# Kernel optimization log

Hardware: AMD Instinct MI355X
Metric: run time of the kernel (lower is better)

Reference implementation:

```python
import jax, jax.numpy as jnp
import numpy as np

B = 16384
EMBED = 1536
DETER = 1024
STOC = 32
HID = 1024
ACT = 12
DIST = 2 * STOC  # mean + std
EPS_LN = 1e-3


def _ln(x, g, b):
    m = jnp.mean(x, axis=-1, keepdims=True)
    v = jnp.mean((x - m) ** 2, axis=-1, keepdims=True)
    return (x - m) * jax.lax.rsqrt(v + EPS_LN) * g + b


def _lin(x, w, b=None):
    y = x @ w.T
    return y if b is None else y + b


def setup_inputs() -> dict:
    key = jax.random.key(0)
    ks = jax.random.split(key, 24)

    def w(k, o, i):
        return jax.random.normal(k, (o, i), jnp.float32) / np.sqrt(i)

    inp = {
        "embedding": jax.random.normal(ks[0], (B, EMBED), jnp.float32),
        "action": jax.random.normal(ks[1], (B, ACT), jnp.float32),
        "mask": jnp.ones((B, 1), jnp.float32),
        "deter": jax.random.normal(ks[2], (B, DETER), jnp.float32),
        "stoc": jax.random.normal(ks[3], (B, STOC), jnp.float32),
        # pre_gru: Linear(stoc+act -> hid)
        "w_pre": w(ks[4], HID, STOC + ACT),
        "b_pre": jnp.zeros((HID,), jnp.float32),
        # NormGRUCell (no bias on ih/hh)
        "w_ih": w(ks[5], 3 * DETER, HID),
        "w_hh": w(ks[6], 3 * DETER, DETER),
        "ln_r_g": jnp.ones((DETER,), jnp.float32), "ln_r_b": jnp.zeros((DETER,), jnp.float32),
        "ln_u_g": jnp.ones((DETER,), jnp.float32), "ln_u_b": jnp.zeros((DETER,), jnp.float32),
        "ln_n_g": jnp.ones((DETER,), jnp.float32), "ln_n_b": jnp.zeros((DETER,), jnp.float32),
        # prior MLP (model_idx = 0)
        "wp1": w(ks[7], HID, DETER), "bp1": jnp.zeros((HID,), jnp.float32),
        "wp2": w(ks[8], DIST, HID), "bp2": jnp.zeros((DIST,), jnp.float32),
        # post MLP
        "wq1": w(ks[9], HID, DETER + EMBED), "bq1": jnp.zeros((HID,), jnp.float32),
        "wq2": w(ks[10], DIST, HID), "bq2": jnp.zeros((DIST,), jnp.float32),
    }
    return inp


def reference(embedding, action, mask, deter, stoc,
              w_pre, b_pre, w_ih, w_hh,
              ln_r_g, ln_r_b, ln_u_g, ln_u_b, ln_n_g, ln_n_b,
              wp1, bp1, wp2, bp2, wq1, bq1, wq2, bq2):
    deter = deter * mask
    stoc = stoc * mask
    x = jax.nn.relu(_lin(jnp.concatenate([stoc, action], -1), w_pre, b_pre))

    # LayerNorm GRU cell
    gi = x @ w_ih.T          # [B, 3*DETER]
    gh = deter @ w_hh.T      # [B, 3*DETER]
    ri, ui, ni = jnp.split(gi, 3, axis=1)
    rh, uh, nh = jnp.split(gh, 3, axis=1)
    reset = jax.nn.sigmoid(_ln(ri + rh, ln_r_g, ln_r_b))
    update = jax.nn.sigmoid(_ln(ui + uh, ln_u_g, ln_u_b))
    newval = jnp.tanh(_ln(ni + reset * nh, ln_n_g, ln_n_b))
    h = update * newval + (1.0 - update) * deter  # [B, DETER]

    # prior head (model 0)
    prior = _lin(jax.nn.relu(_lin(h, wp1, bp1)), wp2, bp2)
    prior_mean, prior_std = jnp.split(prior, 2, axis=-1)
    prior_std = jax.nn.softplus(prior_std) + 0.1

    # posterior head
    post = _lin(jax.nn.relu(_lin(jnp.concatenate([h, embedding], -1), wq1, bq1)), wq2, bq2)
    post_mean, post_std = jnp.split(post, 2, axis=-1)
    post_std = jax.nn.softplus(post_std) + 0.1

    post_latent = post_mean  # sample=False -> Normal mean
    return (post_mean, post_std, prior_mean, prior_std, h, post_latent)
```

## Files before the change

kernel.cpp:

```cpp
#include <hip/hip_runtime.h>
#include <hip/hip_bf16.h>
#include <cstdint>

#define BB 16384

typedef __attribute__((ext_vector_type(8))) short short8;
typedef __attribute__((ext_vector_type(4))) float f32x4;

__device__ __forceinline__ unsigned short f2bf(float x) {
    uint32_t u = __float_as_uint(x);
    u += 0x7FFFu + ((u >> 16) & 1u);
    return (unsigned short)(u >> 16);
}
__device__ __forceinline__ float bf2f(unsigned short b) {
    return __uint_as_float(((uint32_t)b) << 16);
}
__device__ __forceinline__ void split2(float x, unsigned short* hi, unsigned short* lo) {
    unsigned short h = f2bf(x);
    *hi = h;
    *lo = f2bf(x - bf2f(h));
}

#define GLL(gp, lp) __builtin_amdgcn_global_load_lds( \
    (const __attribute__((address_space(1))) void*)(gp), \
    (__attribute__((address_space(3))) void*)(lp), 16, 0, 0)


__global__ __launch_bounds__(256) void split_sa(
    const float* __restrict__ stoc, const float* __restrict__ action,
    const float* __restrict__ mask,
    unsigned short* __restrict__ hi, unsigned short* __restrict__ lo) {
    int tid = threadIdx.x;
    int r = blockIdx.x * 4 + (tid >> 6);
    int c = tid & 63;
    float v = 0.f;
    if (c < 32) v = stoc[(size_t)r * 32 + c] * mask[r];
    else if (c < 44) v = action[(size_t)r * 12 + (c - 32)];
    size_t o = (size_t)r * 64 + c;
    unsigned short h, l; split2(v, &h, &l);
    hi[o] = h; lo[o] = l;
}

__global__ __launch_bounds__(256) void split_wpre(
    const float* __restrict__ w, unsigned short* __restrict__ hi, unsigned short* __restrict__ lo) {
    int idx = blockIdx.x * 256 + threadIdx.x;
    int row = idx >> 6, c = idx & 63;
    float v = (c < 44) ? w[row * 44 + c] : 0.f;
    unsigned short h, l; split2(v, &h, &l);
    hi[idx] = h; lo[idx] = l;
}

__global__ __launch_bounds__(256) void split_weights(
    const float* __restrict__ w0, unsigned short* __restrict__ h0, unsigned short* __restrict__ l0,
    const float* __restrict__ w1, unsigned short* __restrict__ h1, unsigned short* __restrict__ l1,
    const float* __restrict__ w2, unsigned short* __restrict__ h2, unsigned short* __restrict__ l2,
    const float* __restrict__ w3, unsigned short* __restrict__ h3, unsigned short* __restrict__ l3) {
    int b = blockIdx.x;
    const float* src; unsigned short* hi; unsigned short* lo; int lb;
    if (b < 3072)      { src = w0; hi = h0; lo = l0; lb = b; }
    else if (b < 6144) { src = w1; hi = h1; lo = l1; lb = b - 3072; }
    else if (b < 7168) { src = w2; hi = h2; lo = l2; lb = b - 6144; }
    else               { src = w3; hi = h3; lo = l3; lb = b - 7168; }
    size_t i4 = (size_t)lb * 256 + threadIdx.x;
    float4 v = ((const float4*)src)[i4];
    ushort4 h, l;
    split2(v.x, &h.x, &l.x);
    split2(v.y, &h.y, &l.y);
    split2(v.z, &h.z, &l.z);
    split2(v.w, &h.w, &l.w);
    ((ushort4*)hi)[i4] = h;
    ((ushort4*)lo)[i4] = l;
}

__global__ __launch_bounds__(256) void split_embed(
    const float* __restrict__ e, unsigned short* __restrict__ hi, unsigned short* __restrict__ lo) {
    int b = blockIdx.y;
    int c = blockIdx.x * 256 + threadIdx.x;
    float v = e[(size_t)b * 1536 + c];
    size_t o = (size_t)b * 2560 + 1024 + c;
    unsigned short h, l; split2(v, &h, &l);
    hi[o] = h; lo[o] = l;
}

__global__ __launch_bounds__(256) void split_deter(
    const float* __restrict__ dt, const float* __restrict__ mask,
    unsigned short* __restrict__ hi, unsigned short* __restrict__ lo) {
    int b = blockIdx.y;
    int c = blockIdx.x * 256 + threadIdx.x;
    float v = dt[(size_t)b * 1024 + c] * mask[b];
    size_t o = (size_t)b * 1024 + c;
    unsigned short h, l; split2(v, &h, &l);
    hi[o] = h; lo[o] = l;
}

template<int RELU, int BF16OUT, int ACC>
__global__ __launch_bounds__(256, 3) void gemm_hl(
    const unsigned short* __restrict__ Ahi, const unsigned short* __restrict__ Alo, int lda,
    const unsigned short* __restrict__ Bhi, const unsigned short* __restrict__ Blo, int ldb,
    const float* __restrict__ bias,
    float* __restrict__ Cf, unsigned short* __restrict__ Chi, unsigned short* __restrict__ Clo,
    int ldc, int K, int nbn, int gm) {
    __shared__ unsigned short lsAh[128 * 32], lsAl[128 * 32];
    __shared__ unsigned short lsBh[128 * 32], lsBl[128 * 32];

    const int tid = threadIdx.x;
    const int wave = tid >> 6, lane = tid & 63;

    int bid = blockIdx.x;
    int group = bid / (gm * nbn);
    int rem = bid % (gm * nbn);
    int bm = group * gm + (rem % gm);
    int bn = rem / gm;
    const int m0 = bm * 128, n0 = bn * 128;

    const int wm = (wave >> 1) * 64, wn = (wave & 1) * 64;
    const int lr = lane & 15;
    const int ka = (((lane >> 4) ^ ((lane >> 1) & 3)) * 8);

    const int srow = tid >> 2;
    const int scol = (((tid & 3) ^ ((tid >> 3) & 3)) * 8);
    const unsigned short* gA0h = Ahi + (size_t)(m0 + srow) * lda + scol;
    const unsigned short* gA1h = gA0h + (size_t)64 * lda;
    const unsigned short* gA0l = Alo + (size_t)(m0 + srow) * lda + scol;
    const unsigned short* gA1l = gA0l + (size_t)64 * lda;
    const unsigned short* gB0h = Bhi + (size_t)(n0 + srow) * ldb + scol;
    const unsigned short* gB1h = gB0h + (size_t)64 * ldb;
    const unsigned short* gB0l = Blo + (size_t)(n0 + srow) * ldb + scol;
    const unsigned short* gB1l = gB0l + (size_t)64 * ldb;
    const int lds0 = wave * 512;
    const int lds1 = 2048 + wave * 512;

    f32x4 acc[4][4];
    #pragma unroll
    for (int i = 0; i < 4; i++)
        #pragma unroll
        for (int j = 0; j < 4; j++) acc[i][j] = (f32x4){0.f, 0.f, 0.f, 0.f};

    for (int k = 0; k < K; k += 32) {
        __syncthreads();
        GLL(gA0h + k, &lsAh[lds0]);
        GLL(gA1h + k, &lsAh[lds1]);
        GLL(gA0l + k, &lsAl[lds0]);
        GLL(gA1l + k, &lsAl[lds1]);
        GLL(gB0h + k, &lsBh[lds0]);
        GLL(gB1h + k, &lsBh[lds1]);
        GLL(gB0l + k, &lsBl[lds0]);
        GLL(gB1l + k, &lsBl[lds1]);
        __syncthreads();

        short8 a_[4], b_[4], t_[4];
        #pragma unroll
        for (int i = 0; i < 4; i++) {
            a_[i] = *(const short8*)&lsAh[(wm + i * 16 + lr) * 32 + ka];
            b_[i] = *(const short8*)&lsBh[(wn + i * 16 + lr) * 32 + ka];
        }
        #pragma unroll
        for (int i = 0; i < 4; i++)
            #pragma unroll
            for (int j = 0; j < 4; j++)
                acc[i][j] = __builtin_amdgcn_mfma_f32_16x16x32_bf16(a_[i], b_[j], acc[i][j], 0, 0, 0);
        #pragma unroll
        for (int i = 0; i < 4; i++) t_[i] = *(const short8*)&lsBl[(wn + i * 16 + lr) * 32 + ka];
        #pragma unroll
        for (int i = 0; i < 4; i++)
            #pragma unroll
            for (int j = 0; j < 4; j++)
                acc[i][j] = __builtin_amdgcn_mfma_f32_16x16x32_bf16(a_[i], t_[j], acc[i][j], 0, 0, 0);
        #pragma unroll
        for (int i = 0; i < 4; i++) a_[i] = *(const short8*)&lsAl[(wm + i * 16 + lr) * 32 + ka];
        #pragma unroll
        for (int i = 0; i < 4; i++)
            #pragma unroll
            for (int j = 0; j < 4; j++)
                acc[i][j] = __builtin_amdgcn_mfma_f32_16x16x32_bf16(a_[i], b_[j], acc[i][j], 0, 0, 0);
    }

    const int orow = m0 + wm + (lane >> 4) * 4;
    const int ocol = n0 + wn + lr;
    #pragma unroll
    for (int j = 0; j < 4; j++) {
        int col = ocol + j * 16;
        float bv = bias ? bias[col] : 0.f;
        #pragma unroll
        for (int i = 0; i < 4; i++) {
            #pragma unroll
            for (int q = 0; q < 4; q++) {
                int row = orow + i * 16 + q;
                float x = acc[i][j][q] + bv;
                if (ACC) x += Cf[(size_t)row * ldc + col];
                if (RELU) x = fmaxf(x, 0.f);
                if (BF16OUT) {
                    unsigned short h_, l_; split2(x, &h_, &l_);
                    Chi[(size_t)row * ldc + col] = h_;
                    Clo[(size_t)row * ldc + col] = l_;
                } else {
                    Cf[(size_t)row * ldc + col] = x;
                }
            }
        }
    }
}

__device__ __forceinline__ float block_sum(float v, float* red, int tid) {
    #pragma unroll
    for (int m = 32; m >= 1; m >>= 1) v += __shfl_xor(v, m, 64);
    __syncthreads();
    if ((tid & 63) == 0) red[tid >> 6] = v;
    __syncthreads();
    return red[0] + red[1] + red[2] + red[3];
}

__global__ __launch_bounds__(256) void ln_gru(
    const float* __restrict__ gsum, const float* __restrict__ ginb,
    const float* __restrict__ deter, const float* __restrict__ mask,
    const float* __restrict__ grg, const float* __restrict__ grb,
    const float* __restrict__ gug, const float* __restrict__ gub,
    const float* __restrict__ gng, const float* __restrict__ gnb,
    float* __restrict__ hout, unsigned short* __restrict__ hehi, unsigned short* __restrict__ helo) {
    __shared__ float red[4];
    const int b = blockIdx.x, tid = threadIdx.x;
    const float* gr = gsum + (size_t)b * 3072;
    const float mk = mask[b];
    float r[4], u[4], gin[4], ghn[4], dm[4];
    int c[4];
    #pragma unroll
    for (int j = 0; j < 4; j++) {
        c[j] = tid + 256 * j;
        r[j] = gr[c[j]];
        u[j] = gr[1024 + c[j]];
        ghn[j] = gr[2048 + c[j]];
        gin[j] = ginb[(size_t)b * 1024 + c[j]];
        dm[j] = deter[(size_t)b * 1024 + c[j]] * mk;
    }
    const float inv = 1.f / 1024.f;

    float mr = block_sum(r[0] + r[1] + r[2] + r[3], red, tid) * inv;
    float vr;
    {
        float d0 = r[0] - mr, d1 = r[1] - mr, d2 = r[2] - mr, d3 = r[3] - mr;
        vr = block_sum(d0 * d0 + d1 * d1 + d2 * d2 + d3 * d3, red, tid) * inv;
    }
    float sr = rsqrtf(vr + 1e-3f);
    float reset[4];
    #pragma unroll
    for (int j = 0; j < 4; j++) {
        float y = (r[j] - mr) * sr * grg[c[j]] + grb[c[j]];
        reset[j] = 1.f / (1.f + expf(-y));
    }

    float mu = block_sum(u[0] + u[1] + u[2] + u[3], red, tid) * inv;
    float vu;
    {
        float d0 = u[0] - mu, d1 = u[1] - mu, d2 = u[2] - mu, d3 = u[3] - mu;
        vu = block_sum(d0 * d0 + d1 * d1 + d2 * d2 + d3 * d3, red, tid) * inv;
    }
    float su = rsqrtf(vu + 1e-3f);
    float upd[4];
    #pragma unroll
    for (int j = 0; j < 4; j++) {
        float y = (u[j] - mu) * su * gug[c[j]] + gub[c[j]];
        upd[j] = 1.f / (1.f + expf(-y));
    }

    float nin[4];
    #pragma unroll
    for (int j = 0; j < 4; j++) nin[j] = gin[j] + reset[j] * ghn[j];
    float mn = block_sum(nin[0] + nin[1] + nin[2] + nin[3], red, tid) * inv;
    float vn;
    {
        float d0 = nin[0] - mn, d1 = nin[1] - mn, d2 = nin[2] - mn, d3 = nin[3] - mn;
        vn = block_sum(d0 * d0 + d1 * d1 + d2 * d2 + d3 * d3, red, tid) * inv;
    }
    float sn = rsqrtf(vn + 1e-3f);
    #pragma unroll
    for (int j = 0; j < 4; j++) {
        float y = (nin[j] - mn) * sn * gng[c[j]] + gnb[c[j]];
        float nv = tanhf(y);
        float h = upd[j] * nv + (1.f - upd[j]) * dm[j];
        hout[(size_t)b * 1024 + c[j]] = h;
        unsigned short hh, hl; split2(h, &hh, &hl);
        size_t o = (size_t)b * 2560 + c[j];
        hehi[o] = hh;
        helo[o] = hl;
    }
}

__global__ __launch_bounds__(256) void head2(
    const unsigned short* __restrict__ ahi, const unsigned short* __restrict__ alo,
    const float* __restrict__ w, const float* __restrict__ bias,
    float* __restrict__ omean, float* __restrict__ ostd, float* __restrict__ olat) {
    __shared__ float arow[8 * 1024];
    const int tid = threadIdx.x;
    const size_t base = (size_t)blockIdx.x * 8 * 1024;
    for (int i = tid; i < 8 * 1024; i += 256)
        arow[i] = bf2f(ahi[base + i]) + bf2f(alo[base + i]);
    __syncthreads();

    const int j = tid & 63, rq = tid >> 6;
    float acc0 = 0.f, acc1 = 0.f;
    const float* wr = w + (size_t)j * 1024;
    for (int k = 0; k < 1024; k += 4) {
        float4 wv = *(const float4*)(wr + k);
        const float* a0 = &arow[rq * 1024 + k];
        const float* a1 = &arow[(rq + 4) * 1024 + k];
        acc0 += a0[0] * wv.x + a0[1] * wv.y + a0[2] * wv.z + a0[3] * wv.w;
        acc1 += a1[0] * wv.x + a1[1] * wv.y + a1[2] * wv.z + a1[3] * wv.w;
    }
    const float bv = bias[j];
    const int rbase = blockIdx.x * 8;
    float accs[2] = {acc0, acc1};
    #pragma unroll
    for (int t = 0; t < 2; t++) {
        int row = rbase + rq + 4 * t;
        float val = accs[t] + bv;
        if (j < 32) {
            omean[(size_t)row * 32 + j] = val;
            if (olat) olat[(size_t)row * 32 + j] = val;
        } else {
            float sp = fmaxf(val, 0.f) + log1pf(expf(-fabsf(val))) + 0.1f;
            ostd[(size_t)row * 32 + (j - 32)] = sp;
        }
    }
}

static inline size_t rup(size_t x) { return (x + 255) & ~(size_t)255; }

extern "C" void kernel_launch(void* const* d_in, const int* in_sizes, int n_in,
                              void* d_out, int out_size, void* d_ws, size_t ws_size,
                              hipStream_t stream) {
    const float* embedding = (const float*)d_in[0];
    const float* action    = (const float*)d_in[1];
    const float* mask      = (const float*)d_in[2];
    const float* deter     = (const float*)d_in[3];
    const float* stoc      = (const float*)d_in[4];
    const float* w_pre     = (const float*)d_in[5];
    const float* b_pre     = (const float*)d_in[6];
    const float* w_ih      = (const float*)d_in[7];
    const float* w_hh      = (const float*)d_in[8];
    const float* ln_r_g    = (const float*)d_in[9];
    const float* ln_r_b    = (const float*)d_in[10];
    const float* ln_u_g    = (const float*)d_in[11];
    const float* ln_u_b    = (const float*)d_in[12];
    const float* ln_n_g    = (const float*)d_in[13];
    const float* ln_n_b    = (const float*)d_in[14];
    const float* wp1       = (const float*)d_in[15];
    const float* bp1       = (const float*)d_in[16];
    const float* wp2       = (const float*)d_in[17];
    const float* bp2       = (const float*)d_in[18];
    const float* wq1       = (const float*)d_in[19];
    const float* bq1       = (const float*)d_in[20];
    const float* wq2       = (const float*)d_in[21];
    const float* bq2       = (const float*)d_in[22];
    float* out = (float*)d_out;

    const size_t wbytes =
        2 * rup((size_t)65536 * 2) +
        4 * rup((size_t)3072 * 1024 * 2) +
        2 * rup((size_t)1024 * 1024 * 2) +
        2 * rup((size_t)1024 * 2560 * 2);
    int NCH = 16;
    {
        const int cands[5] = {1, 2, 4, 8, 16};
        for (int ci = 0; ci < 5; ci++) {
            size_t Bc = (size_t)BB / cands[ci];
            size_t need = wbytes + Bc * 30976 + (1u << 20);
            if (need <= ws_size) { NCH = cands[ci]; break; }
        }
    }
    const int Bc = BB / NCH;
    const int nbm = Bc / 128;
    const int gm = nbm < 32 ? nbm : 32;

    char* p = (char*)d_ws;
    auto alloc = [&](size_t bytes) { char* r = p; p += rup(bytes); return r; };
    unsigned short* wpre_hi = (unsigned short*)alloc((size_t)65536 * 2);
    unsigned short* wpre_lo = (unsigned short*)alloc((size_t)65536 * 2);
    unsigned short* wih_hi  = (unsigned short*)alloc((size_t)3072 * 1024 * 2);
    unsigned short* wih_lo  = (unsigned short*)alloc((size_t)3072 * 1024 * 2);
    unsigned short* whh_hi  = (unsigned short*)alloc((size_t)3072 * 1024 * 2);
    unsigned short* whh_lo  = (unsigned short*)alloc((size_t)3072 * 1024 * 2);
    unsigned short* wp1_hi  = (unsigned short*)alloc((size_t)1024 * 1024 * 2);
    unsigned short* wp1_lo  = (unsigned short*)alloc((size_t)1024 * 1024 * 2);
    unsigned short* wq1_hi  = (unsigned short*)alloc((size_t)1024 * 2560 * 2);
    unsigned short* wq1_lo  = (unsigned short*)alloc((size_t)1024 * 2560 * 2);
    unsigned short* sa_hi   = (unsigned short*)alloc((size_t)Bc * 64 * 2);
    unsigned short* sa_lo   = (unsigned short*)alloc((size_t)Bc * 64 * 2);
    unsigned short* xh      = (unsigned short*)alloc((size_t)Bc * 1024 * 2);
    unsigned short* xl      = (unsigned short*)alloc((size_t)Bc * 1024 * 2);
    unsigned short* dh      = (unsigned short*)alloc((size_t)Bc * 1024 * 2);
    unsigned short* dl      = (unsigned short*)alloc((size_t)Bc * 1024 * 2);
    float* gh_buf           = (float*)alloc((size_t)Bc * 3072 * 4);
    unsigned short* he_hi   = (unsigned short*)alloc((size_t)Bc * 2560 * 2);
    unsigned short* he_lo   = (unsigned short*)alloc((size_t)Bc * 2560 * 2);
    (void)dl;
    float* gin = (float*)dh;
    unsigned short* p1_hi = (unsigned short*)gh_buf;
    unsigned short* p1_lo = p1_hi + (size_t)Bc * 1024;
    unsigned short* q1_hi = p1_lo + (size_t)Bc * 1024;
    unsigned short* q1_lo = q1_hi + (size_t)Bc * 1024;

    split_wpre<<<256, 256, 0, stream>>>(w_pre, wpre_hi, wpre_lo);
    split_weights<<<9728, 256, 0, stream>>>(
        w_ih, wih_hi, wih_lo, w_hh, whh_hi, whh_lo,
        wp1, wp1_hi, wp1_lo, wq1, wq1_hi, wq1_lo);

    for (int ch = 0; ch < NCH; ch++) {
        const size_t r0 = (size_t)ch * Bc;

        split_sa<<<Bc / 4, 256, 0, stream>>>(
            stoc + r0 * 32, action + r0 * 12, mask + r0, sa_hi, sa_lo);
        split_embed<<<dim3(6, Bc), 256, 0, stream>>>(
            embedding + r0 * 1536, he_hi, he_lo);
        split_deter<<<dim3(4, Bc), 256, 0, stream>>>(
            deter + r0 * 1024, mask + r0, dh, dl);

        gemm_hl<1, 1, 0><<<nbm * 8, 256, 0, stream>>>(
            sa_hi, sa_lo, 64, wpre_hi, wpre_lo, 64, b_pre,
            nullptr, xh, xl, 1024, 64, 8, gm);

        gemm_hl<0, 0, 0><<<nbm * 24, 256, 0, stream>>>(
            dh, dl, 1024, whh_hi, whh_lo, 1024, nullptr,
            gh_buf, nullptr, nullptr, 3072, 1024, 24, gm);

        gemm_hl<0, 0, 1><<<nbm * 16, 256, 0, stream>>>(
            xh, xl, 1024, wih_hi, wih_lo, 1024, nullptr,
            gh_buf, nullptr, nullptr, 3072, 1024, 16, gm);

        gemm_hl<0, 0, 0><<<nbm * 8, 256, 0, stream>>>(
            xh, xl, 1024, wih_hi + (size_t)2048 * 1024, wih_lo + (size_t)2048 * 1024, 1024,
            nullptr, gin, nullptr, nullptr, 1024, 1024, 8, gm);

        ln_gru<<<Bc, 256, 0, stream>>>(
            gh_buf, gin, deter + r0 * 1024, mask + r0,
            ln_r_g, ln_r_b, ln_u_g, ln_u_b, ln_n_g, ln_n_b,
            out + (size_t)BB * 128 + r0 * 1024, he_hi, he_lo);

        gemm_hl<1, 1, 0><<<nbm * 8, 256, 0, stream>>>(
            he_hi, he_lo, 2560, wp1_hi, wp1_lo, 1024, bp1,
            nullptr, p1_hi, p1_lo, 1024, 1024, 8, gm);

        gemm_hl<1, 1, 0><<<nbm * 8, 256, 0, stream>>>(
            he_hi, he_lo, 2560, wq1_hi, wq1_lo, 2560, bq1,
            nullptr, q1_hi, q1_lo, 1024, 2560, 8, gm);

        head2<<<Bc / 8, 256, 0, stream>>>(p1_hi, p1_lo, wp2, bp2,
            out + (size_t)BB * 64 + r0 * 32, out + (size_t)BB * 96 + r0 * 32, nullptr);
        head2<<<Bc / 8, 256, 0, stream>>>(q1_hi, q1_lo, wq2, bq2,
            out + r0 * 32, out + (size_t)BB * 32 + r0 * 32,
            out + (size_t)BB * 1152 + r0 * 32);
    }
}
```

Measured before the change: 1.968 ms.

## Use 256x128 tiles with 8 waves and triple-buffered LDS prefetch pipeline

Replaces the 128x128, 4-wave split-bf16 GEMM with a 256x128 tile run by 8 waves. LDS is triple-buffered, and global-to-LDS loads for step t+2 are issued in between the MFMA phases of step t. Fewer, finer-grained barriers and s_setprio are used around the MFMA blocks so that memory traffic overlaps compute, and the larger tile improves data reuse. The cost is a much larger LDS footprint (about 144KB per block), which limits occupancy. Correctness also depends on the vmcnt bookkeeping being right.

```diff
diff --git a/kernel.cpp b/kernel.cpp
--- a/kernel.cpp
+++ b/kernel.cpp
@@ -94,14 +94,13 @@
 }
 
 template<int RELU, int BF16OUT, int ACC>
-__global__ __launch_bounds__(256, 3) void gemm_hl(
+__global__ __launch_bounds__(512, 2) void gemm_mp(
     const unsigned short* __restrict__ Ahi, const unsigned short* __restrict__ Alo, int lda,
     const unsigned short* __restrict__ Bhi, const unsigned short* __restrict__ Blo, int ldb,
     const float* __restrict__ bias,
     float* __restrict__ Cf, unsigned short* __restrict__ Chi, unsigned short* __restrict__ Clo,
     int ldc, int K, int nbn, int gm) {
-    __shared__ unsigned short lsAh[128 * 32], lsAl[128 * 32];
-    __shared__ unsigned short lsBh[128 * 32], lsBl[128 * 32];
+    __shared__ unsigned short sm[3 * 24576];
 
     const int tid = threadIdx.x;
     const int wave = tid >> 6, lane = tid & 63;
@@ -111,7 +110,7 @@
     int rem = bid % (gm * nbn);
     int bm = group * gm + (rem % gm);
     int bn = rem / gm;
-    const int m0 = bm * 128, n0 = bn * 128;
+    const int m0 = bm * 256, n0 = bn * 128;
 
     const int wm = (wave >> 1) * 64, wn = (wave & 1) * 64;
     const int lr = lane & 15;
@@ -120,15 +119,13 @@
     const int srow = tid >> 2;
     const int scol = (((tid & 3) ^ ((tid >> 3) & 3)) * 8);
     const unsigned short* gA0h = Ahi + (size_t)(m0 + srow) * lda + scol;
-    const unsigned short* gA1h = gA0h + (size_t)64 * lda;
+    const unsigned short* gA1h = gA0h + (size_t)128 * lda;
     const unsigned short* gA0l = Alo + (size_t)(m0 + srow) * lda + scol;
-    const unsigned short* gA1l = gA0l + (size_t)64 * lda;
+    const unsigned short* gA1l = gA0l + (size_t)128 * lda;
     const unsigned short* gB0h = Bhi + (size_t)(n0 + srow) * ldb + scol;
-    const unsigned short* gB1h = gB0h + (size_t)64 * ldb;
     const unsigned short* gB0l = Blo + (size_t)(n0 + srow) * ldb + scol;
-    const unsigned short* gB1l = gB0l + (size_t)64 * ldb;
-    const int lds0 = wave * 512;
-    const int lds1 = 2048 + wave * 512;
+
+    const int wofs = wave * 512;
 
     f32x4 acc[4][4];
     #pragma unroll
@@ -136,43 +133,83 @@
         #pragma unroll
         for (int j = 0; j < 4; j++) acc[i][j] = (f32x4){0.f, 0.f, 0.f, 0.f};
 
-    for (int k = 0; k < K; k += 32) {
-        __syncthreads();
-        GLL(gA0h + k, &lsAh[lds0]);
-        GLL(gA1h + k, &lsAh[lds1]);
-        GLL(gA0l + k, &lsAl[lds0]);
-        GLL(gA1l + k, &lsAl[lds1]);
-        GLL(gB0h + k, &lsBh[lds0]);
-        GLL(gB1h + k, &lsBh[lds1]);
-        GLL(gB0l + k, &lsBl[lds0]);
-        GLL(gB1l + k, &lsBl[lds1]);
-        __syncthreads();
+    const int nt = K >> 5;
+
+    {
+        unsigned short* b0 = sm;
+        unsigned short* b1 = sm + 24576;
+        GLL(gA0h, &b0[wofs]);
+        GLL(gA1h, &b0[4096 + wofs]);
+        GLL(gA0l, &b0[8192 + wofs]);
+        GLL(gA1l, &b0[12288 + wofs]);
+        GLL(gB0h, &b0[16384 + wofs]);
+        GLL(gB0l, &b0[20480 + wofs]);
+        GLL(gA0h + 32, &b1[wofs]);
+        GLL(gA1h + 32, &b1[4096 + wofs]);
+        GLL(gA0l + 32, &b1[8192 + wofs]);
+        GLL(gA1l + 32, &b1[12288 + wofs]);
+        GLL(gB0h + 32, &b1[16384 + wofs]);
+        GLL(gB0l + 32, &b1[20480 + wofs]);
+    }
+
+    int cur = 0;
+    for (int t = 0; t < nt; t++) {
+        if (t + 1 < nt) asm volatile("s_waitcnt vmcnt(6)" ::: "memory");
+        else            asm volatile("s_waitcnt vmcnt(0)" ::: "memory");
+        __builtin_amdgcn_s_barrier();
+
+        unsigned short* cb = sm + cur * 24576;
+        unsigned short* nb = sm + ((cur + 2) % 3) * 24576;
+        const int kpre = (t + 2) * 32;
+        const bool pf = (t + 2) < nt;
 
         short8 a_[4], b_[4], t_[4];
+
         #pragma unroll
         for (int i = 0; i < 4; i++) {
-            a_[i] = *(const short8*)&lsAh[(wm + i * 16 + lr) * 32 + ka];
-            b_[i] = *(const short8*)&lsBh[(wn + i * 16 + lr) * 32 + ka];
+            a_[i] = *(const short8*)&cb[(wm + i * 16 + lr) * 32 + ka];
+            b_[i] = *(const short8*)&cb[16384 + (wn + i * 16 + lr) * 32 + ka];
         }
+        if (pf) { GLL(gA0h + kpre, &nb[wofs]); GLL(gA1h + kpre, &nb[4096 + wofs]); }
+        __builtin_amdgcn_s_barrier();
+        __builtin_amdgcn_s_setprio(1);
         #pragma unroll
         for (int i = 0; i < 4; i++)
             #pragma unroll
             for (int j = 0; j < 4; j++)
                 acc[i][j] = __builtin_amdgcn_mfma_f32_16x16x32_bf16(a_[i], b_[j], acc[i][j], 0, 0, 0);
-        #pragma unroll
-        for (int i = 0; i < 4; i++) t_[i] = *(const short8*)&lsBl[(wn + i * 16 + lr) * 32 + ka];
+        __builtin_amdgcn_s_setprio(0);
+        __builtin_amdgcn_s_barrier();
+
+        #pragma unroll
+        for (int j = 0; j < 4; j++)
+            t_[j] = *(const short8*)&cb[20480 + (wn + j * 16 + lr) * 32 + ka];
+        if (pf) { GLL(gA0l + kpre, &nb[8192 + wofs]); GLL(gA1l + kpre, &nb[12288 + wofs]); }
+        __builtin_amdgcn_s_barrier();
+        __builtin_amdgcn_s_setprio(1);
         #pragma unroll
         for (int i = 0; i < 4; i++)
             #pragma unroll
             for (int j = 0; j < 4; j++)
                 acc[i][j] = __builtin_amdgcn_mfma_f32_16x16x32_bf16(a_[i], t_[j], acc[i][j], 0, 0, 0);
-        #pragma unroll
-        for (int i = 0; i < 4; i++) a_[i] = *(const short8*)&lsAl[(wm + i * 16 + lr) * 32 + ka];
+        __builtin_amdgcn_s_setprio(0);
+        __builtin_amdgcn_s_barrier();
+
+        #pragma unroll
+        for (int i = 0; i < 4; i++)
+            a_[i] = *(const short8*)&cb[8192 + (wm + i * 16 + lr) * 32 + ka];
+        if (pf) { GLL(gB0h + kpre, &nb[16384 + wofs]); GLL(gB0l + kpre, &nb[20480 + wofs]); }
+        __builtin_amdgcn_s_barrier();
+        __builtin_amdgcn_s_setprio(1);
         #pragma unroll
         for (int i = 0; i < 4; i++)
             #pragma unroll
             for (int j = 0; j < 4; j++)
                 acc[i][j] = __builtin_amdgcn_mfma_f32_16x16x32_bf16(a_[i], b_[j], acc[i][j], 0, 0, 0);
+        __builtin_amdgcn_s_setprio(0);
+        __builtin_amdgcn_s_barrier();
+
+        cur = (cur + 1) % 3;
     }
 
     const int orow = m0 + wm + (lane >> 4) * 4;
@@ -368,8 +405,8 @@
         }
     }
     const int Bc = BB / NCH;
-    const int nbm = Bc / 128;
-    const int gm = nbm < 32 ? nbm : 32;
+    const int nbm = Bc / 256;
+    const int gm = nbm < 16 ? nbm : 16;
 
     char* p = (char*)d_ws;
     auto alloc = [&](size_t bytes) { char* r = p; p += rup(bytes); return r; };
@@ -414,19 +451,19 @@
         split_deter<<<dim3(4, Bc), 256, 0, stream>>>(
             deter + r0 * 1024, mask + r0, dh, dl);
 
-        gemm_hl<1, 1, 0><<<nbm * 8, 256, 0, stream>>>(
+        gemm_mp<1, 1, 0><<<nbm * 8, 512, 0, stream>>>(
             sa_hi, sa_lo, 64, wpre_hi, wpre_lo, 64, b_pre,
             nullptr, xh, xl, 1024, 64, 8, gm);
 
-        gemm_hl<0, 0, 0><<<nbm * 24, 256, 0, stream>>>(
+        gemm_mp<0, 0, 0><<<nbm * 24, 512, 0, stream>>>(
             dh, dl, 1024, whh_hi, whh_lo, 1024, nullptr,
             gh_buf, nullptr, nullptr, 3072, 1024, 24, gm);
 
-        gemm_hl<0, 0, 1><<<nbm * 16, 256, 0, stream>>>(
+        gemm_mp<0, 0, 1><<<nbm * 16, 512, 0, stream>>>(
             xh, xl, 1024, wih_hi, wih_lo, 1024, nullptr,
             gh_buf, nullptr, nullptr, 3072, 1024, 16, gm);
 
-        gemm_hl<0, 0, 0><<<nbm * 8, 256, 0, stream>>>(
+        gemm_mp<0, 0, 0><<<nbm * 8, 512, 0, stream>>>(
             xh, xl, 1024, wih_hi + (size_t)2048 * 1024, wih_lo + (size_t)2048 * 1024, 1024,
             nullptr, gin, nullptr, nullptr, 1024, 1024, 8, gm);
 
@@ -435,11 +472,11 @@
             ln_r_g, ln_r_b, ln_u_g, ln_u_b, ln_n_g, ln_n_b,
             out + (size_t)BB * 128 + r0 * 1024, he_hi, he_lo);
 
-        gemm_hl<1, 1, 0><<<nbm * 8, 256, 0, stream>>>(
+        gemm_mp<1, 1, 0><<<nbm * 8, 512, 0, stream>>>(
             he_hi, he_lo, 2560, wp1_hi, wp1_lo, 1024, bp1,
             nullptr, p1_hi, p1_lo, 1024, 1024, 8, gm);
 
-        gemm_hl<1, 1, 0><<<nbm * 8, 256, 0, stream>>>(
+        gemm_mp<1, 1, 0><<<nbm * 8, 512, 0, stream>>>(
             he_hi, he_lo, 2560, wq1_hi, wq1_lo, 2560, bq1,
             nullptr, q1_hi, q1_lo, 1024, 2560, 8, gm);
 
```

Result: faster. 1.873 ms (-4.8%).
